# Optimization experiments

Hardware: AMD Instinct MI355X
Metric: run time of the kernel (lower is better)

The kernel has to match this reference:

```python
import jax, jax.numpy as jnp
import numpy as np

B, P, F = 256, 361, 20  # batch, channel pairs, frequency bins


def setup_inputs() -> dict:
    key = jax.random.key(0)
    ks = jax.random.split(key, 32)
    r = lambda i, shape, s=0.05: jax.random.normal(ks[i], shape, jnp.float32) * s
    return {
        "x": jax.random.normal(ks[0], (B, P, F, 2), jnp.float32),
        # 20 independent real-branch MLPs: 1 -> 16 -> 32 -> 32 (stacked over freq axis)
        "rw1": r(1, (F, 16)), "rb1": r(2, (F, 16)),
        "rw2": r(3, (F, 16, 32)), "rb2": r(4, (F, 32)),
        "rw3": r(5, (F, 32, 32)), "rb3": r(6, (F, 32)),
        # 20 independent imag-branch MLPs
        "iw1": r(7, (F, 16)), "ib1": r(8, (F, 16)),
        "iw2": r(9, (F, 16, 32)), "ib2": r(10, (F, 32)),
        "iw3": r(11, (F, 32, 32)), "ib3": r(12, (F, 32)),
        # 20 fusion layers: 64 -> 32 -> 32
        "fw1": r(13, (F, 64, 32)), "fb1": r(14, (F, 32)),
        "fw2": r(15, (F, 32, 32)), "fb2": r(16, (F, 32)),
        # frequency processor: importance weights + MLP 20 -> 64 -> 64 -> 32
        "freq_imp": jnp.ones((F,), jnp.float32),
        "pw1": r(17, (F, 64)), "pb1": r(18, (64,)),
        "pw2": r(19, (64, 64)), "pb2": r(20, (64,)),
        "pw3": r(21, (64, 32)), "pb3": r(22, (32,)),
        # final fusion: 64 -> 128 -> 64
        "gw1": r(23, (64, 128)), "gb1": r(24, (128,)),
        "gw2": r(25, (128, 64)), "gb2": r(26, (64,)),
    }


def _gelu(v):
    return jax.nn.gelu(v, approximate=False)  # matches torch nn.GELU default


def _branch(v, w1, b1, w2, b2, w3, b3):
    # v: (B,P,F) scalar input per freq; 20 independent MLPs batched via einsum
    h = _gelu(v[..., None] * w1 + b1)                      # (B,P,F,16)
    h = _gelu(jnp.einsum('bpfh,fhk->bpfk', h, w2) + b2)    # (B,P,F,32)
    return jnp.einsum('bpfh,fhk->bpfk', h, w3) + b3        # (B,P,F,32)


def reference(x, rw1, rb1, rw2, rb2, rw3, rb3,
              iw1, ib1, iw2, ib2, iw3, ib3,
              fw1, fb1, fw2, fb2,
              freq_imp, pw1, pb1, pw2, pb2, pw3, pb3,
              gw1, gb1, gw2, gb2):
    real, imag = x[..., 0], x[..., 1]                      # (B,P,F)
    ro = _branch(real, rw1, rb1, rw2, rb2, rw3, rb3)       # (B,P,F,32)
    io = _branch(imag, iw1, ib1, iw2, ib2, iw3, ib3)       # (B,P,F,32)
    cat = jnp.concatenate([ro, io], axis=-1)               # (B,P,F,64)
    h = _gelu(jnp.einsum('bpfh,fhk->bpfk', cat, fw1) + fb1)
    complex_features = jnp.einsum('bpfh,fhk->bpfk', h, fw2) + fb2  # (B,P,F,32)
    aggregated = complex_features.mean(axis=2)             # (B,P,32), freq_aggregation='mean'
    # frequency branch: magnitude of complex pair, importance-weighted MLP
    mag = jnp.sqrt(real * real + imag * imag + 1e-8)       # (B,P,F)
    w = jax.nn.softmax(freq_imp)
    fh = _gelu((mag * w) @ pw1 + pb1)                      # (B,P,64)
    fh = _gelu(fh @ pw2 + pb2)
    freq_features = fh @ pw3 + pb3                         # (B,P,32)
    u = jnp.concatenate([freq_features, aggregated], axis=-1)  # (B,P,64)
    h = _gelu(u @ gw1 + gb1)
    return h @ gw2 + gb2                                   # (B,P,64)
```

## Files before the change

kernel.cpp:

```cpp
#include <hip/hip_runtime.h>
#include <math.h>

#define Bv 256
#define Pv 361
#define Fv 20
#define NROW (Bv*Pv)

__device__ __forceinline__ float gelu_f(float z){
    const float y  = z * 0.70710678118654752440f;
    const float ax = fabsf(y);
    const float t  = __builtin_amdgcn_rcpf(fmaf(0.3275911f, ax, 1.0f));
    float p = fmaf(1.061405429f, t, -1.453152027f);
    p = fmaf(p, t, 1.421413741f);
    p = fmaf(p, t, -0.284496736f);
    p = fmaf(p, t, 0.254829592f);
    p *= t;
    const float e = __expf(-y*y);
    float er = fmaf(-p, e, 1.0f);
    er = copysignf(er, y);
    return 0.5f * z * (1.0f + er);
}

template<int N>
__device__ __forceinline__ void gelu_v(float* __restrict__ v){
    #pragma unroll
    for (int i = 0; i < N; ++i) v[i] = gelu_f(v[i]);
}

__device__ __forceinline__ void cpb4(float* dst, const float* __restrict__ src, int nfl){
    const float4* s = (const float4*)src;
    float4* d = (float4*)dst;
    for (int i = threadIdx.x; i < (nfl >> 2); i += 256) d[i] = s[i];
}

template<int NIN, int NOUT>
__device__ __forceinline__ void dense(const float* __restrict__ sm, int wbase, int bbase,
                                      const float* __restrict__ in, float* __restrict__ out){
    #pragma unroll
    for (int k = 0; k < NOUT; ++k) out[k] = sm[bbase + k];
    #pragma unroll
    for (int i = 0; i < NIN; ++i){
        const float a = in[i];
        const float4* w = (const float4*)&sm[wbase + i*NOUT];
        #pragma unroll
        for (int k4 = 0; k4 < NOUT/4; ++k4){
            float4 ww = w[k4];
            out[4*k4+0] = fmaf(a, ww.x, out[4*k4+0]);
            out[4*k4+1] = fmaf(a, ww.y, out[4*k4+1]);
            out[4*k4+2] = fmaf(a, ww.z, out[4*k4+2]);
            out[4*k4+3] = fmaf(a, ww.w, out[4*k4+3]);
        }
    }
}

template<int NIN, int NOUT>
__device__ __forceinline__ void dense_acc(const float* __restrict__ sm, int wbase,
                                          const float* __restrict__ in, float* __restrict__ out){
    #pragma unroll
    for (int i = 0; i < NIN; ++i){
        const float a = in[i];
        const float4* w = (const float4*)&sm[wbase + i*NOUT];
        #pragma unroll
        for (int k4 = 0; k4 < NOUT/4; ++k4){
            float4 ww = w[k4];
            out[4*k4+0] = fmaf(a, ww.x, out[4*k4+0]);
            out[4*k4+1] = fmaf(a, ww.y, out[4*k4+1]);
            out[4*k4+2] = fmaf(a, ww.z, out[4*k4+2]);
            out[4*k4+3] = fmaf(a, ww.w, out[4*k4+3]);
        }
    }
}

#define BST 1632
#define OW1 0
#define OB1 16
#define OW2 32
#define OB2 544
#define OW3T 576
#define OB3 1600
#define OFW1 3264
#define OFB1 5312
#define OFW2 5344
#define OFB2 6368

__global__ __launch_bounds__(256, 2) void k_branch(
    const float* __restrict__ x,
    const float* __restrict__ rw1, const float* __restrict__ rb1,
    const float* __restrict__ rw2, const float* __restrict__ rb2,
    const float* __restrict__ rw3, const float* __restrict__ rb3,
    const float* __restrict__ iw1, const float* __restrict__ ib1,
    const float* __restrict__ iw2, const float* __restrict__ ib2,
    const float* __restrict__ iw3, const float* __restrict__ ib3,
    const float* __restrict__ fw1, const float* __restrict__ fb1,
    const float* __restrict__ fw2, const float* __restrict__ fb2,
    float* __restrict__ partial, int nf)
{
    __shared__ __align__(16) float sm[6400];
    const int tid = threadIdx.x;
    const int row = blockIdx.x * 256 + tid;
    const int g   = blockIdx.y;
    const float2* __restrict__ x2 = (const float2*)x;

    float acc[32];
    #pragma unroll
    for (int k = 0; k < 32; ++k) acc[k] = 0.f;

    #pragma unroll 1
    for (int ff = 0; ff < nf; ++ff){
        const int f = g*nf + ff;
        __syncthreads();
        cpb4(sm+0*BST+OW1, rw1+f*16,  16);  cpb4(sm+0*BST+OB1, rb1+f*16,  16);
        cpb4(sm+0*BST+OW2, rw2+f*512, 512); cpb4(sm+0*BST+OB2, rb2+f*32,  32);
        cpb4(sm+0*BST+OB3, rb3+f*32,  32);
        cpb4(sm+1*BST+OW1, iw1+f*16,  16);  cpb4(sm+1*BST+OB1, ib1+f*16,  16);
        cpb4(sm+1*BST+OW2, iw2+f*512, 512); cpb4(sm+1*BST+OB2, ib2+f*32,  32);
        cpb4(sm+1*BST+OB3, ib3+f*32,  32);
        for (int t = tid; t < 1024; t += 256){
            sm[0*BST+OW3T+t] = rw3[f*1024 + (t&31)*32 + (t>>5)];
            sm[1*BST+OW3T+t] = iw3[f*1024 + (t&31)*32 + (t>>5)];
        }
        cpb4(sm+OFW1, fw1+f*2048, 2048); cpb4(sm+OFB1, fb1+f*32, 32);
        cpb4(sm+OFW2, fw2+f*1024, 1024); cpb4(sm+OFB2, fb2+f*32, 32);
        __syncthreads();

        const float2 xv = x2[(size_t)row*Fv + f];

        float hf[32];
        #pragma unroll
        for (int k = 0; k < 32; ++k) hf[k] = sm[OFB1+k];

        #pragma unroll 1
        for (int br = 0; br < 2; ++br){
            const int wb = br*BST;
            const float xb = br ? xv.y : xv.x;
            float h1[16];
            #pragma unroll
            for (int i = 0; i < 16; ++i)
                h1[i] = gelu_f(fmaf(xb, sm[wb+OW1+i], sm[wb+OB1+i]));
            float h2[32];
            dense<16,32>(sm, wb+OW2, wb+OB2, h1, h2);
            gelu_v<32>(h2);
            #pragma unroll 1
            for (int i = 0; i < 32; ++i){
                const float4* wt = (const float4*)&sm[wb + OW3T + i*32];
                float d0=0.f, d1=0.f, d2=0.f, d3=0.f;
                #pragma unroll
                for (int k4 = 0; k4 < 8; ++k4){
                    float4 ww = wt[k4];
                    d0 = fmaf(h2[4*k4+0], ww.x, d0);
                    d1 = fmaf(h2[4*k4+1], ww.y, d1);
                    d2 = fmaf(h2[4*k4+2], ww.z, d2);
                    d3 = fmaf(h2[4*k4+3], ww.w, d3);
                }
                const float oi = sm[wb + OB3 + i] + ((d0+d1)+(d2+d3));
                const float4* wf = (const float4*)&sm[OFW1 + (br*32 + i)*32];
                #pragma unroll
                for (int k4 = 0; k4 < 8; ++k4){
                    float4 ww = wf[k4];
                    hf[4*k4+0] = fmaf(oi, ww.x, hf[4*k4+0]);
                    hf[4*k4+1] = fmaf(oi, ww.y, hf[4*k4+1]);
                    hf[4*k4+2] = fmaf(oi, ww.z, hf[4*k4+2]);
                    hf[4*k4+3] = fmaf(oi, ww.w, hf[4*k4+3]);
                }
            }
        }
        gelu_v<32>(hf);
        #pragma unroll
        for (int k = 0; k < 32; ++k) acc[k] += sm[OFB2+k];
        dense_acc<32,32>(sm, OFW2, hf, acc);
    }

    float4* o = (float4*)(partial + ((size_t)g*NROW + row)*32);
    #pragma unroll
    for (int k4 = 0; k4 < 8; ++k4)
        o[k4] = make_float4(acc[4*k4+0], acc[4*k4+1], acc[4*k4+2], acc[4*k4+3]);
}

__global__ __launch_bounds__(256, 2) void k_tail(
    const float* __restrict__ x,
    const float* __restrict__ freq_imp,
    const float* __restrict__ pw1, const float* __restrict__ pb1,
    const float* __restrict__ pw2, const float* __restrict__ pb2,
    const float* __restrict__ pw3, const float* __restrict__ pb3,
    const float* __restrict__ gw1, const float* __restrict__ gb1,
    const float* __restrict__ gw2, const float* __restrict__ gb2,
    const float* __restrict__ partial, int ng,
    float* __restrict__ out)
{
    __shared__ __align__(16) float sm[16576];
    const int tid = threadIdx.x;
    const int row = blockIdx.x * 256 + tid;

    float w[20];
    float mx = -1e30f;
    #pragma unroll
    for (int f = 0; f < 20; ++f){ w[f] = freq_imp[f]; mx = fmaxf(mx, w[f]); }
    float s = 0.f;
    #pragma unroll
    for (int f = 0; f < 20; ++f){ w[f] = __expf(w[f]-mx); s += w[f]; }
    const float inv = __builtin_amdgcn_rcpf(s);
    float mw[20];
    const float2* __restrict__ xr = (const float2*)x + (size_t)row*Fv;
    #pragma unroll
    for (int f = 0; f < 20; ++f){
        float2 v = xr[f];
        mw[f] = sqrtf(fmaf(v.x,v.x, fmaf(v.y,v.y, 1e-8f))) * (w[f]*inv);
    }

    enum { PW1=0, PB1=1280, PW2T=1344, PB2=5440, PW3=5504, PB3=7552 };
    cpb4(sm+PW1, pw1, 1280); cpb4(sm+PB1, pb1, 64);
    for (int t = tid; t < 4096; t += 256)
        sm[PW2T + t] = pw2[(t&63)*64 + (t>>6)];
    cpb4(sm+PB2, pb2, 64);
    cpb4(sm+PW3, pw3, 2048); cpb4(sm+PB3, pb3, 32);
    __syncthreads();

    float t1[64];
    dense<20,64>(sm, PW1, PB1, mw, t1);
    gelu_v<64>(t1);

    float ffr[32];
    #pragma unroll
    for (int k = 0; k < 32; ++k) ffr[k] = sm[PB3+k];
    #pragma unroll 1
    for (int i = 0; i < 64; ++i){
        const float4* wt = (const float4*)&sm[PW2T + i*64];
        float d0=0.f, d1=0.f, d2=0.f, d3=0.f;
        #pragma unroll
        for (int k4 = 0; k4 < 16; ++k4){
            float4 ww = wt[k4];
            d0 = fmaf(t1[4*k4+0], ww.x, d0);
            d1 = fmaf(t1[4*k4+1], ww.y, d1);
            d2 = fmaf(t1[4*k4+2], ww.z, d2);
            d3 = fmaf(t1[4*k4+3], ww.w, d3);
        }
        const float t2i = gelu_f(sm[PB2+i] + ((d0+d1)+(d2+d3)));
        const float4* wp = (const float4*)&sm[PW3 + i*32];
        #pragma unroll
        for (int k4 = 0; k4 < 8; ++k4){
            float4 ww = wp[k4];
            ffr[4*k4+0] = fmaf(t2i, ww.x, ffr[4*k4+0]);
            ffr[4*k4+1] = fmaf(t2i, ww.y, ffr[4*k4+1]);
            ffr[4*k4+2] = fmaf(t2i, ww.z, ffr[4*k4+2]);
            ffr[4*k4+3] = fmaf(t2i, ww.w, ffr[4*k4+3]);
        }
    }
    __syncthreads();

    float acc[32];
    #pragma unroll
    for (int k = 0; k < 32; ++k) acc[k] = 0.f;
    #pragma unroll 1
    for (int g = 0; g < ng; ++g){
        const float4* pg = (const float4*)(partial + ((size_t)g*NROW + row)*32);
        #pragma unroll
        for (int k4 = 0; k4 < 8; ++k4){
            float4 v = pg[k4];
            acc[4*k4+0] += v.x; acc[4*k4+1] += v.y;
            acc[4*k4+2] += v.z; acc[4*k4+3] += v.w;
        }
    }
    #pragma unroll
    for (int k = 0; k < 32; ++k) acc[k] *= (1.f/20.f);

    enum { GW1T=0, GB1=8192, GW2=8320, GB2=16512 };
    for (int t = tid; t < 8192; t += 256)
        sm[GW1T + t] = gw1[(t&63)*128 + (t>>6)];
    cpb4(sm+GB1, gb1, 128); cpb4(sm+GW2, gw2, 8192); cpb4(sm+GB2, gb2, 64);
    __syncthreads();

    #pragma unroll 1
    for (int half = 0; half < 2; ++half){
        float o[32];
        #pragma unroll
        for (int k = 0; k < 32; ++k) o[k] = sm[GB2 + half*32 + k];
        #pragma unroll 1
        for (int j = 0; j < 128; ++j){
            const float4* wv = (const float4*)&sm[GW1T + j*64];
            float d0=0.f, d1=0.f, d2=0.f, d3=0.f;
            #pragma unroll
            for (int i4 = 0; i4 < 8; ++i4){
                float4 ww = wv[i4];
                d0 = fmaf(ffr[4*i4+0], ww.x, d0);
                d1 = fmaf(ffr[4*i4+1], ww.y, d1);
                d2 = fmaf(ffr[4*i4+2], ww.z, d2);
                d3 = fmaf(ffr[4*i4+3], ww.w, d3);
            }
            #pragma unroll
            for (int i4 = 0; i4 < 8; ++i4){
                float4 ww = wv[8+i4];
                d0 = fmaf(acc[4*i4+0], ww.x, d0);
                d1 = fmaf(acc[4*i4+1], ww.y, d1);
                d2 = fmaf(acc[4*i4+2], ww.z, d2);
                d3 = fmaf(acc[4*i4+3], ww.w, d3);
            }
            const float d = gelu_f(sm[GB1+j] + ((d0+d1)+(d2+d3)));
            const float4* w2 = (const float4*)&sm[GW2 + j*64 + half*32];
            #pragma unroll
            for (int k4 = 0; k4 < 8; ++k4){
                float4 ww = w2[k4];
                o[4*k4+0] = fmaf(d, ww.x, o[4*k4+0]);
                o[4*k4+1] = fmaf(d, ww.y, o[4*k4+1]);
                o[4*k4+2] = fmaf(d, ww.z, o[4*k4+2]);
                o[4*k4+3] = fmaf(d, ww.w, o[4*k4+3]);
            }
        }
        float4* op = (float4*)(out + (size_t)row*64 + half*32);
        #pragma unroll
        for (int k4 = 0; k4 < 8; ++k4)
            op[k4] = make_float4(o[4*k4+0], o[4*k4+1], o[4*k4+2], o[4*k4+3]);
    }
}

extern "C" void kernel_launch(void* const* d_in, const int* in_sizes, int n_in,
                              void* d_out, int out_size, void* d_ws, size_t ws_size,
                              hipStream_t stream) {
    (void)in_sizes; (void)n_in; (void)out_size;
    const float* x   = (const float*)d_in[0];
    const float* rw1 = (const float*)d_in[1];  const float* rb1 = (const float*)d_in[2];
    const float* rw2 = (const float*)d_in[3];  const float* rb2 = (const float*)d_in[4];
    const float* rw3 = (const float*)d_in[5];  const float* rb3 = (const float*)d_in[6];
    const float* iw1 = (const float*)d_in[7];  const float* ib1 = (const float*)d_in[8];
    const float* iw2 = (const float*)d_in[9];  const float* ib2 = (const float*)d_in[10];
    const float* iw3 = (const float*)d_in[11]; const float* ib3 = (const float*)d_in[12];
    const float* fw1 = (const float*)d_in[13]; const float* fb1 = (const float*)d_in[14];
    const float* fw2 = (const float*)d_in[15]; const float* fb2 = (const float*)d_in[16];
    const float* fim = (const float*)d_in[17];
    const float* pw1 = (const float*)d_in[18]; const float* pb1 = (const float*)d_in[19];
    const float* pw2 = (const float*)d_in[20]; const float* pb2 = (const float*)d_in[21];
    const float* pw3 = (const float*)d_in[22]; const float* pb3 = (const float*)d_in[23];
    const float* gw1 = (const float*)d_in[24]; const float* gb1 = (const float*)d_in[25];
    const float* gw2 = (const float*)d_in[26]; const float* gb2 = (const float*)d_in[27];
    float* out = (float*)d_out;
    float* partial = (float*)d_ws;

    const size_t per = (size_t)NROW * 32 * sizeof(float);
    int ng;
    if      (ws_size >= 5*per) ng = 5;
    else if (ws_size >= 4*per) ng = 4;
    else if (ws_size >= 2*per) ng = 2;
    else                       ng = 1;
    const int nf = Fv / ng;

    dim3 g1(361, ng);
    hipLaunchKernelGGL(k_branch, g1, dim3(256), 0, stream,
                       x, rw1, rb1, rw2, rb2, rw3, rb3,
                       iw1, ib1, iw2, ib2, iw3, ib3,
                       fw1, fb1, fw2, fb2, partial, nf);
    hipLaunchKernelGGL(k_tail, dim3(361), dim3(256), 0, stream,
                       x, fim, pw1, pb1, pw2, pb2, pw3, pb3,
                       gw1, gb1, gw2, gb2, partial, ng, out);
}
```

Baseline: 901.5 us.

## Double-buffer per-frequency weights in LDS and pad transposed weight tiles

The branch kernel now keeps two LDS weight buffers and stages the next frequency's weights while computing the current one, which drops one barrier per iteration. It also loads the transposed w3, pw2 and gw1 matrices with coalesced float4 global reads and writes them into padded strides (36/68) to reduce LDS bank conflicts on the scatter. The tail kernel moves a barrier so the partial-sum reduction overlaps the previous LDS use. The cost is roughly double the LDS per block in k_branch (about 53 KB), which may limit how many blocks fit per CU.

Result: no change. 885.1 us (-1.8%).

```diff
diff --git a/kernel.cpp b/kernel.cpp
--- a/kernel.cpp
+++ b/kernel.cpp
@@ -71,17 +71,36 @@
     }
 }
 
-#define BST 1632
-#define OW1 0
-#define OB1 16
-#define OW2 32
-#define OB2 544
+#define BST  1760
+#define OW1  0
+#define OB1  16
+#define OW2  32
+#define OB2  544
 #define OW3T 576
-#define OB3 1600
-#define OFW1 3264
-#define OFB1 5312
-#define OFW2 5344
-#define OFB2 6368
+#define OB3  1728
+#define OFW1 3520
+#define OFB1 5568
+#define OFW2 5600
+#define OFB2 6624
+#define BUFSZ 6656
+
+__device__ __forceinline__ void stage_branch(float* b, int f, int tid,
+    const float* __restrict__ w1, const float* __restrict__ b1,
+    const float* __restrict__ w2, const float* __restrict__ b2,
+    const float* __restrict__ w3, const float* __restrict__ b3){
+    cpb4(b+OW1, w1+f*16,  16);
+    cpb4(b+OB1, b1+f*16,  16);
+    cpb4(b+OW2, w2+f*512, 512);
+    cpb4(b+OB2, b2+f*32,  32);
+    cpb4(b+OB3, b3+f*32,  32);
+    {
+        const float4 v = *(const float4*)&w3[f*1024 + tid*4];
+        const int t = tid*4; const int k = t>>5; const int i0 = t&31;
+        float* dst = b + OW3T + k;
+        dst[(i0+0)*36] = v.x; dst[(i0+1)*36] = v.y;
+        dst[(i0+2)*36] = v.z; dst[(i0+3)*36] = v.w;
+    }
+}
 
 __global__ __launch_bounds__(256, 2) void k_branch(
     const float* __restrict__ x,
@@ -95,7 +114,7 @@
     const float* __restrict__ fw2, const float* __restrict__ fb2,
     float* __restrict__ partial, int nf)
 {
-    __shared__ __align__(16) float sm[6400];
+    __shared__ __align__(16) float sm[2*BUFSZ];
     const int tid = threadIdx.x;
     const int row = blockIdx.x * 256 + tid;
     const int g   = blockIdx.y;
@@ -105,29 +124,34 @@
     #pragma unroll
     for (int k = 0; k < 32; ++k) acc[k] = 0.f;
 
+    float* ba = sm;
+    float* bb = sm + BUFSZ;
+
+    {
+        const int f0 = g*nf;
+        stage_branch(ba+0,   f0, tid, rw1,rb1,rw2,rb2,rw3,rb3);
+        stage_branch(ba+BST, f0, tid, iw1,ib1,iw2,ib2,iw3,ib3);
+        cpb4(ba+OFW1, fw1+f0*2048, 2048); cpb4(ba+OFB1, fb1+f0*32, 32);
+        cpb4(ba+OFW2, fw2+f0*1024, 1024); cpb4(ba+OFB2, fb2+f0*32, 32);
+    }
+    __syncthreads();
+
     #pragma unroll 1
     for (int ff = 0; ff < nf; ++ff){
         const int f = g*nf + ff;
-        __syncthreads();
-        cpb4(sm+0*BST+OW1, rw1+f*16,  16);  cpb4(sm+0*BST+OB1, rb1+f*16,  16);
-        cpb4(sm+0*BST+OW2, rw2+f*512, 512); cpb4(sm+0*BST+OB2, rb2+f*32,  32);
-        cpb4(sm+0*BST+OB3, rb3+f*32,  32);
-        cpb4(sm+1*BST+OW1, iw1+f*16,  16);  cpb4(sm+1*BST+OB1, ib1+f*16,  16);
-        cpb4(sm+1*BST+OW2, iw2+f*512, 512); cpb4(sm+1*BST+OB2, ib2+f*32,  32);
-        cpb4(sm+1*BST+OB3, ib3+f*32,  32);
-        for (int t = tid; t < 1024; t += 256){
-            sm[0*BST+OW3T+t] = rw3[f*1024 + (t&31)*32 + (t>>5)];
-            sm[1*BST+OW3T+t] = iw3[f*1024 + (t&31)*32 + (t>>5)];
-        }
-        cpb4(sm+OFW1, fw1+f*2048, 2048); cpb4(sm+OFB1, fb1+f*32, 32);
-        cpb4(sm+OFW2, fw2+f*1024, 1024); cpb4(sm+OFB2, fb2+f*32, 32);
-        __syncthreads();
+        if (ff + 1 < nf){
+            const int fn = f + 1;
+            stage_branch(bb+0,   fn, tid, rw1,rb1,rw2,rb2,rw3,rb3);
+            stage_branch(bb+BST, fn, tid, iw1,ib1,iw2,ib2,iw3,ib3);
+            cpb4(bb+OFW1, fw1+fn*2048, 2048); cpb4(bb+OFB1, fb1+fn*32, 32);
+            cpb4(bb+OFW2, fw2+fn*1024, 1024); cpb4(bb+OFB2, fb2+fn*32, 32);
+        }
 
         const float2 xv = x2[(size_t)row*Fv + f];
 
         float hf[32];
         #pragma unroll
-        for (int k = 0; k < 32; ++k) hf[k] = sm[OFB1+k];
+        for (int k = 0; k < 32; ++k) hf[k] = ba[OFB1+k];
 
         #pragma unroll 1
         for (int br = 0; br < 2; ++br){
@@ -136,13 +160,13 @@
             float h1[16];
             #pragma unroll
             for (int i = 0; i < 16; ++i)
-                h1[i] = gelu_f(fmaf(xb, sm[wb+OW1+i], sm[wb+OB1+i]));
+                h1[i] = gelu_f(fmaf(xb, ba[wb+OW1+i], ba[wb+OB1+i]));
             float h2[32];
-            dense<16,32>(sm, wb+OW2, wb+OB2, h1, h2);
+            dense<16,32>(ba, wb+OW2, wb+OB2, h1, h2);
             gelu_v<32>(h2);
             #pragma unroll 1
             for (int i = 0; i < 32; ++i){
-                const float4* wt = (const float4*)&sm[wb + OW3T + i*32];
+                const float4* wt = (const float4*)&ba[wb + OW3T + i*36];
                 float d0=0.f, d1=0.f, d2=0.f, d3=0.f;
                 #pragma unroll
                 for (int k4 = 0; k4 < 8; ++k4){
@@ -152,8 +176,8 @@
                     d2 = fmaf(h2[4*k4+2], ww.z, d2);
                     d3 = fmaf(h2[4*k4+3], ww.w, d3);
                 }
-                const float oi = sm[wb + OB3 + i] + ((d0+d1)+(d2+d3));
-                const float4* wf = (const float4*)&sm[OFW1 + (br*32 + i)*32];
+                const float oi = ba[wb + OB3 + i] + ((d0+d1)+(d2+d3));
+                const float4* wf = (const float4*)&ba[OFW1 + (br*32 + i)*32];
                 #pragma unroll
                 for (int k4 = 0; k4 < 8; ++k4){
                     float4 ww = wf[k4];
@@ -166,8 +190,11 @@
         }
         gelu_v<32>(hf);
         #pragma unroll
-        for (int k = 0; k < 32; ++k) acc[k] += sm[OFB2+k];
-        dense_acc<32,32>(sm, OFW2, hf, acc);
+        for (int k = 0; k < 32; ++k) acc[k] += ba[OFB2+k];
+        dense_acc<32,32>(ba, OFW2, hf, acc);
+
+        __syncthreads();
+        float* tmp = ba; ba = bb; bb = tmp;
     }
 
     float4* o = (float4*)(partial + ((size_t)g*NROW + row)*32);
@@ -187,7 +214,7 @@
     const float* __restrict__ partial, int ng,
     float* __restrict__ out)
 {
-    __shared__ __align__(16) float sm[16576];
+    __shared__ __align__(16) float sm[17088];
     const int tid = threadIdx.x;
     const int row = blockIdx.x * 256 + tid;
 
@@ -207,10 +234,14 @@
         mw[f] = sqrtf(fmaf(v.x,v.x, fmaf(v.y,v.y, 1e-8f))) * (w[f]*inv);
     }
 
-    enum { PW1=0, PB1=1280, PW2T=1344, PB2=5440, PW3=5504, PB3=7552 };
+    enum { PW1=0, PB1=1280, PW2T=1344, PB2=5696, PW3=5760, PB3=7808 };
     cpb4(sm+PW1, pw1, 1280); cpb4(sm+PB1, pb1, 64);
-    for (int t = tid; t < 4096; t += 256)
-        sm[PW2T + t] = pw2[(t&63)*64 + (t>>6)];
+    for (int t4 = tid; t4 < 1024; t4 += 256){
+        float4 v = ((const float4*)pw2)[t4];
+        int t = t4*4; int k = t>>6; int i0 = t&63;
+        float* dst = sm + PW2T + k;
+        dst[(i0+0)*68]=v.x; dst[(i0+1)*68]=v.y; dst[(i0+2)*68]=v.z; dst[(i0+3)*68]=v.w;
+    }
     cpb4(sm+PB2, pb2, 64);
     cpb4(sm+PW3, pw3, 2048); cpb4(sm+PB3, pb3, 32);
     __syncthreads();
@@ -224,7 +255,7 @@
     for (int k = 0; k < 32; ++k) ffr[k] = sm[PB3+k];
     #pragma unroll 1
     for (int i = 0; i < 64; ++i){
-        const float4* wt = (const float4*)&sm[PW2T + i*64];
+        const float4* wt = (const float4*)&sm[PW2T + i*68];
         float d0=0.f, d1=0.f, d2=0.f, d3=0.f;
         #pragma unroll
         for (int k4 = 0; k4 < 16; ++k4){
@@ -245,7 +276,6 @@
             ffr[4*k4+3] = fmaf(t2i, ww.w, ffr[4*k4+3]);
         }
     }
-    __syncthreads();
 
     float acc[32];
     #pragma unroll
@@ -262,10 +292,15 @@
     }
     #pragma unroll
     for (int k = 0; k < 32; ++k) acc[k] *= (1.f/20.f);
-
-    enum { GW1T=0, GB1=8192, GW2=8320, GB2=16512 };
-    for (int t = tid; t < 8192; t += 256)
-        sm[GW1T + t] = gw1[(t&63)*128 + (t>>6)];
+    __syncthreads();
+
+    enum { GW1T=0, GB1=8704, GW2=8832, GB2=17024 };
+    for (int t4 = tid; t4 < 2048; t4 += 256){
+        float4 v = ((const float4*)gw1)[t4];
+        int t = t4*4; int i = t>>7; int j0 = t&127;
+        float* dst = sm + GW1T + i;
+        dst[(j0+0)*68]=v.x; dst[(j0+1)*68]=v.y; dst[(j0+2)*68]=v.z; dst[(j0+3)*68]=v.w;
+    }
     cpb4(sm+GB1, gb1, 128); cpb4(sm+GW2, gw2, 8192); cpb4(sm+GB2, gb2, 64);
     __syncthreads();
 
@@ -276,7 +311,7 @@
         for (int k = 0; k < 32; ++k) o[k] = sm[GB2 + half*32 + k];
         #pragma unroll 1
         for (int j = 0; j < 128; ++j){
-            const float4* wv = (const float4*)&sm[GW1T + j*64];
+            const float4* wv = (const float4*)&sm[GW1T + j*68];
             float d0=0.f, d1=0.f, d2=0.f, d3=0.f;
             #pragma unroll
             for (int i4 = 0; i4 < 8; ++i4){
```
